# Kernel optimization log

Hardware: AMD Instinct MI355X
Metric: run time of the kernel (lower is better)

The kernel has to match this reference:

```python
import jax, jax.numpy as jnp
import numpy as np

N_NODES = 50000
N_EDGES = 800000
FIN = 128
FQK = 128
FV = 128
H = 8


def setup_inputs() -> dict:
    key = jax.random.key(0)
    k1, k2, k3, k4, k5 = jax.random.split(key, 5)
    x = jax.random.normal(k1, (N_NODES, FIN), dtype=jnp.float32)
    # nn.Linear(Fin, 2*Fqk+Fv, bias=False): weight shape [Ftot, Fin]
    W = jax.random.normal(k2, (2 * FQK + FV, FIN), dtype=jnp.float32) / np.sqrt(FIN)
    # src must be sorted (scatter_* assume batch[-1]+1 segments)
    src = jnp.sort(jax.random.randint(k3, (N_EDGES,), 0, N_NODES))
    dest = jax.random.randint(k4, (N_EDGES,), 0, N_NODES)
    ei = jnp.stack([src, dest])
    batch = jnp.sort(jax.random.randint(k5, (N_NODES,), 0, 64))
    return {"x": x, "W": W, "batch": batch, "ei": ei}


def reference(x, W, batch, ei):
    n = x.shape[0]
    Fh = FQK // H    # 16
    Fhv = FV // H    # 16
    scaling = float(Fh) ** (-0.5)
    src, dest = ei[0], ei[1]

    qkv = x @ W.T                                   # [n, 2*Fqk+Fv]
    q = (qkv[:, :FQK] * scaling).reshape(n, H, Fh)
    k = qkv[:, FQK:2 * FQK].reshape(n, H, Fh)
    v = qkv[:, 2 * FQK:].reshape(n, H, Fhv)

    # per-edge attention scores, one per head: [E, H]
    aw = jnp.einsum('ehf,ehf->eh', q[src], k[dest])
    # faithful to original scatter_softmax: subtract GLOBAL per-head max
    aw = aw - aw.max(axis=0)
    ex = jnp.exp(aw)
    denom = jax.ops.segment_sum(ex, src, num_segments=n)[src]   # [E, H]
    a = ex / denom

    out = jax.ops.segment_sum(a[:, :, None] * v[dest], src, num_segments=n)  # [n, H, Fhv]
    return out.reshape(n, H * Fhv)
```

## Files before the change

kernel.cpp:

```cpp
#include <hip/hip_runtime.h>
#include <hip/hip_fp16.h>
#include <math.h>

#define FIN_ 128

typedef _Float16 half2v __attribute__((ext_vector_type(2)));
typedef _Float16 half8v __attribute__((ext_vector_type(8)));
typedef __attribute__((ext_vector_type(4))) float float4v;

__device__ __forceinline__ half2v u2h(unsigned u) {
    union { unsigned u; half2v h; } c; c.u = u; return c.h;
}

__global__ __launch_bounds__(256) void cvt_and_rowptr(const float* __restrict__ x,
                                                      const float* __restrict__ W,
                                                      _Float16* __restrict__ xh,
                                                      _Float16* __restrict__ wh,
                                                      const int* __restrict__ src,
                                                      int* __restrict__ rowptr,
                                                      int nx8, int nw8, int nE, int n) {
    int i = blockIdx.x * blockDim.x + threadIdx.x;
    if (i < nx8 + nw8) {
        const float* s;
        _Float16* d;
        if (i < nx8) { s = x + (size_t)i * 8; d = xh + (size_t)i * 8; }
        else { s = W + (size_t)(i - nx8) * 8; d = wh + (size_t)(i - nx8) * 8; }
        const float4 a = *(const float4*)s;
        const float4 b = *(const float4*)(s + 4);
        half8v r;
        r[0] = (_Float16)a.x; r[1] = (_Float16)a.y;
        r[2] = (_Float16)a.z; r[3] = (_Float16)a.w;
        r[4] = (_Float16)b.x; r[5] = (_Float16)b.y;
        r[6] = (_Float16)b.z; r[7] = (_Float16)b.w;
        *(half8v*)d = r;
    } else {
        const int j = i - (nx8 + nw8);
        if (j > n) return;
        int lo = 0, hi = nE;
        while (lo < hi) {
            int mid = (lo + hi) >> 1;
            if (src[mid] < j) lo = mid + 1; else hi = mid;
        }
        rowptr[j] = lo;
    }
}

__global__ __launch_bounds__(256) void gemm_qkv_mfma(const _Float16* __restrict__ xh,
                                                     const _Float16* __restrict__ wh,
                                                     _Float16* __restrict__ qb,
                                                     _Float16* __restrict__ kv,
                                                     int n) {
    __shared__ _Float16 smem[2 * 128 * 68];
    _Float16 (*xs)[68] = (_Float16(*)[68])smem;
    _Float16 (*ws)[68] = (_Float16(*)[68])(smem + 128 * 68);
    const int row0 = blockIdx.x * 128;
    const int f0   = blockIdx.y * 128;
    const int t = threadIdx.x;
    const int lane = t & 63;
    const int wave = t >> 6;
    const int wr = wave >> 1, wc = wave & 1;
    const int l15 = lane & 15, kg = lane >> 4;

    float4v acc[4][4];
#pragma unroll
    for (int i = 0; i < 4; ++i)
#pragma unroll
        for (int j = 0; j < 4; ++j) acc[i][j] = (float4v)0.f;

    const int r5 = t >> 3;
    const int c8 = (t & 7) * 8;

    for (int half = 0; half < 2; ++half) {
        __syncthreads();
#pragma unroll
        for (int p = 0; p < 4; ++p) {
            const int row = p * 32 + r5;
            const int gxr = row0 + row;
            half8v vx = (half8v)(_Float16)0;
            if (gxr < n) vx = *(const half8v*)(xh + (size_t)gxr * FIN_ + half * 64 + c8);
            *(half8v*)&xs[row][c8] = vx;
            *(half8v*)&ws[row][c8] =
                *(const half8v*)(wh + (size_t)(f0 + row) * FIN_ + half * 64 + c8);
        }
        __syncthreads();
#pragma unroll
        for (int ks = 0; ks < 2; ++ks) {
            const int kcol = ks * 32 + kg * 8;
            half8v a[4], b[4];
#pragma unroll
            for (int mi = 0; mi < 4; ++mi)
                a[mi] = *(half8v*)&ws[wr * 64 + mi * 16 + l15][kcol];
#pragma unroll
            for (int ni = 0; ni < 4; ++ni)
                b[ni] = *(half8v*)&xs[wc * 64 + ni * 16 + l15][kcol];
#pragma unroll
            for (int mi = 0; mi < 4; ++mi)
#pragma unroll
                for (int ni = 0; ni < 4; ++ni)
                    acc[mi][ni] = __builtin_amdgcn_mfma_f32_16x16x32_f16(
                        a[mi], b[ni], acc[mi][ni], 0, 0, 0);
        }
    }

    __syncthreads();
    _Float16 (*T)[136] = (_Float16(*)[136])smem;
    const bool isq = (f0 == 0);
    const float s = isq ? 0.25f : 1.0f;
#pragma unroll
    for (int mi = 0; mi < 4; ++mi) {
        const int fb = wr * 64 + mi * 16 + kg * 4;
#pragma unroll
        for (int ni = 0; ni < 4; ++ni) {
            const int nl = wc * 64 + ni * 16 + l15;
            union { ushort4 u; _Float16 f[4]; } pk;
#pragma unroll
            for (int r = 0; r < 4; ++r) pk.f[r] = (_Float16)(acc[mi][ni][r] * s);
            *(ushort4*)&T[nl][fb] = pk.u;
        }
    }
    __syncthreads();
#pragma unroll
    for (int i = 0; i < 8; ++i) {
        const int u = t + i * 256;
        const int nl = u >> 4;
        const int cs = (u & 15) * 8;
        const int ng = row0 + nl;
        if (ng >= n) continue;
        const half8v val = *(const half8v*)&T[nl][cs];
        if (isq) *(half8v*)&qb[(size_t)ng * 128 + cs] = val;
        else     *(half8v*)&kv[(size_t)ng * 256 + (f0 - 128) + cs] = val;
    }
}

__device__ __forceinline__ float dot16(uint4 k0, uint4 k1, const half2v* q) {
#if __has_builtin(__builtin_amdgcn_fdot2)
    float s = __builtin_amdgcn_fdot2(u2h(k0.x), q[0], 0.f, false);
    s = __builtin_amdgcn_fdot2(u2h(k0.y), q[1], s, false);
    s = __builtin_amdgcn_fdot2(u2h(k0.z), q[2], s, false);
    s = __builtin_amdgcn_fdot2(u2h(k0.w), q[3], s, false);
    s = __builtin_amdgcn_fdot2(u2h(k1.x), q[4], s, false);
    s = __builtin_amdgcn_fdot2(u2h(k1.y), q[5], s, false);
    s = __builtin_amdgcn_fdot2(u2h(k1.z), q[6], s, false);
    s = __builtin_amdgcn_fdot2(u2h(k1.w), q[7], s, false);
    return s;
#else
    half2v a = u2h(k0.x) * q[0];
    a += u2h(k0.y) * q[1];
    a += u2h(k0.z) * q[2];
    a += u2h(k0.w) * q[3];
    a += u2h(k1.x) * q[4];
    a += u2h(k1.y) * q[5];
    a += u2h(k1.z) * q[6];
    a += u2h(k1.w) * q[7];
    return (float)a[0] + (float)a[1];
#endif
}

__global__ __launch_bounds__(256) void attn_edges_ep(const _Float16* __restrict__ qb,
                                                     const _Float16* __restrict__ kv,
                                                     const int* __restrict__ rowptr,
                                                     const int* __restrict__ dest,
                                                     float* __restrict__ out, int n) {
    const int wave = threadIdx.x >> 6;
    const int node = blockIdx.x * 4 + wave;
    if (node >= n) return;
    const int lane = threadIdx.x & 63;
    const int j = lane >> 3;
    const int h = lane & 7;
    const int ppos = ((j & 1) << 3) | ((j & 2) << 1) | ((j & 4) >> 1);
    float* outp = &out[(size_t)node * FIN_ + h * 16 + ppos];

    const int e0 = rowptr[node];
    const int e1 = rowptr[node + 1];
    if (e0 == e1) {
        *(float2*)outp = make_float2(0.f, 0.f);
        return;
    }

    half2v qh[8];
    {
        const uint4 q0 = *(const uint4*)(qb + (size_t)node * 128 + h * 16);
        const uint4 q1 = *(const uint4*)(qb + (size_t)node * 128 + h * 16 + 8);
        qh[0] = u2h(q0.x); qh[1] = u2h(q0.y); qh[2] = u2h(q0.z); qh[3] = u2h(q0.w);
        qh[4] = u2h(q1.x); qh[5] = u2h(q1.y); qh[6] = u2h(q1.z); qh[7] = u2h(q1.w);
    }

    float lsum = 0.f;
    half2v a8[8];
#pragma unroll
    for (int i = 0; i < 8; ++i) a8[i] = (half2v)(_Float16)0;

    const int hoff = h << 4;
    for (int eb = e0; eb < e1; eb += 16) {
        const int eA = eb + j;
        const int eB = eb + 8 + j;
        const bool vA = eA < e1;
        const bool vB = eB < e1;
        const unsigned dA = (unsigned)dest[vA ? eA : (e1 - 1)];
        const unsigned dB = (unsigned)dest[vB ? eB : (e1 - 1)];
        const unsigned offA = (dA << 8) + hoff;
        const unsigned offB = (dB << 8) + hoff;
        const uint4 k0A = *(const uint4*)(kv + offA);
        const uint4 k1A = *(const uint4*)(kv + offA + 8);
        const uint4 v0A = *(const uint4*)(kv + offA + 128);
        const uint4 v1A = *(const uint4*)(kv + offA + 136);
        const uint4 k0B = *(const uint4*)(kv + offB);
        const uint4 k1B = *(const uint4*)(kv + offB + 8);
        const uint4 v0B = *(const uint4*)(kv + offB + 128);
        const uint4 v1B = *(const uint4*)(kv + offB + 136);

        const float sA = dot16(k0A, k1A, qh);
        const float sB = dot16(k0B, k1B, qh);
        const float pA = vA ? __expf(sA) : 0.f;
        const float pB = vB ? __expf(sB) : 0.f;
        lsum += pA + pB;

        const _Float16 ha = (_Float16)pA, hb = (_Float16)pB;
        const half2v pa = {ha, ha}, pb = {hb, hb};
        a8[0] += pa * u2h(v0A.x) + pb * u2h(v0B.x);
        a8[1] += pa * u2h(v0A.y) + pb * u2h(v0B.y);
        a8[2] += pa * u2h(v0A.z) + pb * u2h(v0B.z);
        a8[3] += pa * u2h(v0A.w) + pb * u2h(v0B.w);
        a8[4] += pa * u2h(v1A.x) + pb * u2h(v1B.x);
        a8[5] += pa * u2h(v1A.y) + pb * u2h(v1B.y);
        a8[6] += pa * u2h(v1A.z) + pb * u2h(v1B.z);
        a8[7] += pa * u2h(v1A.w) + pb * u2h(v1B.w);
    }

    lsum += __shfl_xor(lsum, 8);
    lsum += __shfl_xor(lsum, 16);
    lsum += __shfl_xor(lsum, 32);

    float a16[16];
#pragma unroll
    for (int i = 0; i < 8; ++i) {
        a16[2 * i]     = (float)a8[i][0];
        a16[2 * i + 1] = (float)a8[i][1];
    }

    float r8[8];
    {
        const bool b = (j & 1) != 0;
#pragma unroll
        for (int i = 0; i < 8; ++i) {
            const float keep = b ? a16[i + 8] : a16[i];
            const float send = b ? a16[i] : a16[i + 8];
            r8[i] = keep + __shfl_xor(send, 8);
        }
    }
    float r4[4];
    {
        const bool b = (j & 2) != 0;
#pragma unroll
        for (int i = 0; i < 4; ++i) {
            const float keep = b ? r8[i + 4] : r8[i];
            const float send = b ? r8[i] : r8[i + 4];
            r4[i] = keep + __shfl_xor(send, 16);
        }
    }
    float r2[2];
    {
        const bool b = (j & 4) != 0;
#pragma unroll
        for (int i = 0; i < 2; ++i) {
            const float keep = b ? r4[i + 2] : r4[i];
            const float send = b ? r4[i] : r4[i + 2];
            r2[i] = keep + __shfl_xor(send, 32);
        }
    }

    const float inv = (lsum > 0.f) ? 1.f / lsum : 0.f;
    *(float2*)outp = make_float2(r2[0] * inv, r2[1] * inv);
}

extern "C" void kernel_launch(void* const* d_in, const int* in_sizes, int n_in,
                              void* d_out, int out_size, void* d_ws, size_t ws_size,
                              hipStream_t stream) {
    const float* x = (const float*)d_in[0];
    const float* W = (const float*)d_in[1];
    const int* ei = (const int*)d_in[3];

    const int n = in_sizes[0] / FIN_;
    const int nW = in_sizes[1];
    const int nE = in_sizes[3] / 2;
    const int* src = ei;
    const int* dest = ei + nE;

    char* w = (char*)d_ws;
    _Float16* qb = (_Float16*)w;   w += (size_t)n * 128 * 2;
    _Float16* kv = (_Float16*)w;   w += (size_t)n * 256 * 2;
    int* rowptr = (int*)w;         w += ((size_t)(n + 1) * 4 + 15) & ~(size_t)15;
    _Float16* xh = (_Float16*)w;   w += (size_t)n * FIN_ * 2;
    _Float16* wh = (_Float16*)w;
    float* out = (float*)d_out;

    const int nx8 = n * FIN_ / 8, nw8 = nW / 8;
    const int tot = nx8 + nw8 + n + 1;
    cvt_and_rowptr<<<(tot + 255) / 256, 256, 0, stream>>>(x, W, xh, wh, src, rowptr,
                                                          nx8, nw8, nE, n);

    dim3 g1((n + 127) / 128, 3);
    gemm_qkv_mfma<<<g1, 256, 0, stream>>>(xh, wh, qb, kv, n);

    attn_edges_ep<<<(n + 3) / 4, 256, 0, stream>>>(qb, kv, rowptr, dest, out, n);
}
```

Baseline: 102.7 us.

## Load GEMM MFMA operands directly from global memory and prescale W for q

The QKV GEMM no longer stages x and W tiles through shared memory with barriers. Each lane now loads its MFMA fragments straight from global memory, relying on the cache for reuse. The q scaling factor is folded into the fp16 conversion of W's first 128 rows, which removes a multiply in the epilogue. This cuts LDS traffic and synchronisation but issues more redundant global or L2 loads, and the W scaling slightly changes fp16 rounding.

Measured after the change: 96.32 us. 1.07x faster.

```diff
diff --git a/kernel.cpp b/kernel.cpp
--- a/kernel.cpp
+++ b/kernel.cpp
@@ -23,15 +23,20 @@
     if (i < nx8 + nw8) {
         const float* s;
         _Float16* d;
+        float sc = 1.0f;
         if (i < nx8) { s = x + (size_t)i * 8; d = xh + (size_t)i * 8; }
-        else { s = W + (size_t)(i - nx8) * 8; d = wh + (size_t)(i - nx8) * 8; }
+        else {
+            const int k = i - nx8;
+            if ((k >> 4) < 128) sc = 0.25f;
+            s = W + (size_t)k * 8; d = wh + (size_t)k * 8;
+        }
         const float4 a = *(const float4*)s;
         const float4 b = *(const float4*)(s + 4);
         half8v r;
-        r[0] = (_Float16)a.x; r[1] = (_Float16)a.y;
-        r[2] = (_Float16)a.z; r[3] = (_Float16)a.w;
-        r[4] = (_Float16)b.x; r[5] = (_Float16)b.y;
-        r[6] = (_Float16)b.z; r[7] = (_Float16)b.w;
+        r[0] = (_Float16)(a.x * sc); r[1] = (_Float16)(a.y * sc);
+        r[2] = (_Float16)(a.z * sc); r[3] = (_Float16)(a.w * sc);
+        r[4] = (_Float16)(b.x * sc); r[5] = (_Float16)(b.y * sc);
+        r[6] = (_Float16)(b.z * sc); r[7] = (_Float16)(b.w * sc);
         *(half8v*)d = r;
     } else {
         const int j = i - (nx8 + nw8);
@@ -50,9 +55,7 @@
                                                      _Float16* __restrict__ qb,
                                                      _Float16* __restrict__ kv,
                                                      int n) {
-    __shared__ _Float16 smem[2 * 128 * 68];
-    _Float16 (*xs)[68] = (_Float16(*)[68])smem;
-    _Float16 (*ws)[68] = (_Float16(*)[68])(smem + 128 * 68);
+    __shared__ _Float16 T[128][136];
     const int row0 = blockIdx.x * 128;
     const int f0   = blockIdx.y * 128;
     const int t = threadIdx.x;
@@ -67,32 +70,26 @@
 #pragma unroll
         for (int j = 0; j < 4; ++j) acc[i][j] = (float4v)0.f;
 
-    const int r5 = t >> 3;
-    const int c8 = (t & 7) * 8;
-
+    int nodeIdx[4];
+#pragma unroll
+    for (int ni = 0; ni < 4; ++ni) {
+        const int nd = row0 + wc * 64 + ni * 16 + l15;
+        nodeIdx[ni] = (nd < n) ? nd : 0;
+    }
+    const size_t fbase = (size_t)(f0 + wr * 64 + l15) * FIN_;
+
+#pragma unroll
     for (int half = 0; half < 2; ++half) {
-        __syncthreads();
-#pragma unroll
-        for (int p = 0; p < 4; ++p) {
-            const int row = p * 32 + r5;
-            const int gxr = row0 + row;
-            half8v vx = (half8v)(_Float16)0;
-            if (gxr < n) vx = *(const half8v*)(xh + (size_t)gxr * FIN_ + half * 64 + c8);
-            *(half8v*)&xs[row][c8] = vx;
-            *(half8v*)&ws[row][c8] =
-                *(const half8v*)(wh + (size_t)(f0 + row) * FIN_ + half * 64 + c8);
-        }
-        __syncthreads();
 #pragma unroll
         for (int ks = 0; ks < 2; ++ks) {
-            const int kcol = ks * 32 + kg * 8;
+            const int koff = half * 64 + ks * 32 + kg * 8;
             half8v a[4], b[4];
 #pragma unroll
             for (int mi = 0; mi < 4; ++mi)
-                a[mi] = *(half8v*)&ws[wr * 64 + mi * 16 + l15][kcol];
+                a[mi] = *(const half8v*)(wh + fbase + (size_t)mi * 16 * FIN_ + koff);
 #pragma unroll
             for (int ni = 0; ni < 4; ++ni)
-                b[ni] = *(half8v*)&xs[wc * 64 + ni * 16 + l15][kcol];
+                b[ni] = *(const half8v*)(xh + (size_t)nodeIdx[ni] * FIN_ + koff);
 #pragma unroll
             for (int mi = 0; mi < 4; ++mi)
 #pragma unroll
@@ -102,10 +99,6 @@
         }
     }
 
-    __syncthreads();
-    _Float16 (*T)[136] = (_Float16(*)[136])smem;
-    const bool isq = (f0 == 0);
-    const float s = isq ? 0.25f : 1.0f;
 #pragma unroll
     for (int mi = 0; mi < 4; ++mi) {
         const int fb = wr * 64 + mi * 16 + kg * 4;
@@ -114,11 +107,12 @@
             const int nl = wc * 64 + ni * 16 + l15;
             union { ushort4 u; _Float16 f[4]; } pk;
 #pragma unroll
-            for (int r = 0; r < 4; ++r) pk.f[r] = (_Float16)(acc[mi][ni][r] * s);
+            for (int r = 0; r < 4; ++r) pk.f[r] = (_Float16)acc[mi][ni][r];
             *(ushort4*)&T[nl][fb] = pk.u;
         }
     }
     __syncthreads();
+    const bool isq = (f0 == 0);
 #pragma unroll
     for (int i = 0; i < 8; ++i) {
         const int u = t + i * 256;
```
